# Optimization experiments

Measured on AMD Instinct MI355X. Metric: run time of the kernel, lower is better.

The kernel has to match this reference:

```python
import jax, jax.numpy as jnp
import numpy as np

# Fixed 15-joint skeleton: parent joint index for each keypoint (from build()).
LIMB_CONNECTION = jnp.array([0, 0, 1, 1, 1, 3, 4, 5, 6, 2, 2, 9, 10, 11, 12], dtype=jnp.int32)


def setup_inputs() -> dict:
    key = jax.random.key(0)
    B, K, D = 500000, 15, 3
    inputs = jax.random.normal(key, (B, K, D), dtype=jnp.float32)
    return {"inputs": inputs}


def reference(inputs) -> jnp.ndarray:
    # inputs: [B, K, D]; gather parent keypoints via limb_connection, then
    # Euclidean distance per (b, kp). Output [B, K, 1] as in the original.
    parents = inputs[:, LIMB_CONNECTION, :]            # [B, K, D]
    diff = inputs - parents                            # [B, K, D]
    limbs = jnp.sqrt(jnp.sum(diff * diff, axis=-1))    # [B, K]
    return limbs[:, :, None]                           # [B, K, 1]
```

## Files before the change

### kernel.cpp

```cpp
#include <hip/hip_runtime.h>


#define LIMB_PACK 0x0CBA922654311100ULL

__global__ __launch_bounds__(256) void limb_length_kernel(
    const float* __restrict__ in, float* __restrict__ out, int total) {
    int tid = blockIdx.x * blockDim.x + threadIdx.x;
    if (tid >= total) return;

    unsigned ut = (unsigned)tid;
    unsigned b = ut / 15u;
    unsigned k = ut - b * 15u;
    unsigned p = (unsigned)((LIMB_PACK >> (k * 4u)) & 0xFULL);

    const float* __restrict__ row = in + (size_t)b * 45u;
    float x0 = row[k * 3u + 0u];
    float y0 = row[k * 3u + 1u];
    float z0 = row[k * 3u + 2u];
    float x1 = row[p * 3u + 0u];
    float y1 = row[p * 3u + 1u];
    float z1 = row[p * 3u + 2u];

    float dx = x0 - x1;
    float dy = y0 - y1;
    float dz = z0 - z1;
    out[tid] = sqrtf(dx * dx + dy * dy + dz * dz);
}

extern "C" void kernel_launch(void* const* d_in, const int* in_sizes, int n_in,
                              void* d_out, int out_size, void* d_ws, size_t ws_size,
                              hipStream_t stream) {
    const float* in = (const float*)d_in[0];
    float* out = (float*)d_out;
    int total = out_size;
    int block = 256;
    int grid = (total + block - 1) / block;
    limb_length_kernel<<<grid, block, 0, stream>>>(in, out, total);
}
```

Baseline: 135.6 us.

## Stage body rows in LDS via coalesced float4 nontemporal loads

Each 960-thread block loads 64 bodies (2880 floats) into shared memory with coalesced 16-byte nontemporal loads, then computes limb lengths from LDS and writes the outputs with nontemporal stores. This replaces the strided, redundant scalar global gathers of the parent and child joints. The cost is a block-wide barrier and large blocks, which may limit occupancy. The tail relies on the total input size being a multiple of 4 floats.

```diff
diff --git a/kernel.cpp b/kernel.cpp
--- a/kernel.cpp
+++ b/kernel.cpp
@@ -1,39 +1,54 @@
 #include <hip/hip_runtime.h>
 
 
+typedef float f32x4 __attribute__((ext_vector_type(4)));
+
 #define LIMB_PACK 0x0CBA922654311100ULL
 
-__global__ __launch_bounds__(256) void limb_length_kernel(
-    const float* __restrict__ in, float* __restrict__ out, int total) {
-    int tid = blockIdx.x * blockDim.x + threadIdx.x;
-    if (tid >= total) return;
+#define BODIES_PER_BLOCK 64
+#define BLOCK_THREADS    960
+#define F4_PER_BLOCK     720
 
-    unsigned ut = (unsigned)tid;
-    unsigned b = ut / 15u;
-    unsigned k = ut - b * 15u;
-    unsigned p = (unsigned)((LIMB_PACK >> (k * 4u)) & 0xFULL);
+__global__ __launch_bounds__(BLOCK_THREADS) void limb_length_v2(
+    const f32x4* __restrict__ in4, float* __restrict__ out,
+    int n_body, int n_float4) {
+    __shared__ float lds[BODIES_PER_BLOCK * 45];
 
-    const float* __restrict__ row = in + (size_t)b * 45u;
-    float x0 = row[k * 3u + 0u];
-    float y0 = row[k * 3u + 1u];
-    float z0 = row[k * 3u + 2u];
-    float x1 = row[p * 3u + 0u];
-    float y1 = row[p * 3u + 1u];
-    float z1 = row[p * 3u + 2u];
+    const int tid = threadIdx.x;
+    const int blk = blockIdx.x;
 
-    float dx = x0 - x1;
-    float dy = y0 - y1;
-    float dz = z0 - z1;
-    out[tid] = sqrtf(dx * dx + dy * dy + dz * dz);
+    if (tid < F4_PER_BLOCK) {
+        int gi = blk * F4_PER_BLOCK + tid;
+        if (gi < n_float4) {
+            f32x4 v = __builtin_nontemporal_load(&in4[gi]);
+            ((f32x4*)lds)[tid] = v;
+        }
+    }
+    __syncthreads();
+
+    const unsigned ut = (unsigned)tid;
+    const unsigned lb = ut / 15u;
+    const unsigned k  = ut - lb * 15u;
+    const int body = blk * BODIES_PER_BLOCK + (int)lb;
+    if (body >= n_body) return;
+
+    const unsigned p = (unsigned)((LIMB_PACK >> (k * 4u)) & 0xFULL);
+    const float* __restrict__ row = lds + lb * 45u;
+    const float dx = row[k * 3u + 0u] - row[p * 3u + 0u];
+    const float dy = row[k * 3u + 1u] - row[p * 3u + 1u];
+    const float dz = row[k * 3u + 2u] - row[p * 3u + 2u];
+
+    __builtin_nontemporal_store(sqrtf(dx * dx + dy * dy + dz * dz),
+                                &out[blk * BLOCK_THREADS + tid]);
 }
 
 extern "C" void kernel_launch(void* const* d_in, const int* in_sizes, int n_in,
                               void* d_out, int out_size, void* d_ws, size_t ws_size,
                               hipStream_t stream) {
-    const float* in = (const float*)d_in[0];
+    const f32x4* in4 = (const f32x4*)d_in[0];
     float* out = (float*)d_out;
-    int total = out_size;
-    int block = 256;
-    int grid = (total + block - 1) / block;
-    limb_length_kernel<<<grid, block, 0, stream>>>(in, out, total);
+    const int n_body = out_size / 15;
+    const int n_float4 = in_sizes[0] / 4;
+    const int grid = (n_body + BODIES_PER_BLOCK - 1) / BODIES_PER_BLOCK;
+    limb_length_v2<<<grid, BLOCK_THREADS, 0, stream>>>(in4, out, n_body, n_float4);
 }
```

New measurement: 137.6 us. No clear change (+1.5%).
